# Optimization experiments

Measured on AMD Instinct MI355X. Metric: run time of the kernel, lower is better.

## Reference

```python
import jax, jax.numpy as jnp
from jax import lax
import numpy as np

NUM_NODES = 4
C = 256
P = 64
TOTAL_EDGES = sum(n + 1 for n in range(NUM_NODES))  # 10
STRENGTH = 1.0
W_SCALE = 0.02  # scale on raw randn weights to keep cascaded convs numerically tame


def setup_inputs() -> dict:
    key = jax.random.key(0)
    ks = jax.random.split(key, 16)
    rng = np.random.default_rng(0)
    idx = jnp.asarray(
        np.stack([rng.permutation(C)[:P] for _ in range(TOTAL_EDGES)]), dtype=jnp.int32
    )
    return {
        "x": jax.random.normal(ks[0], (64, C, 32, 32), jnp.float32),
        "arch_params": jax.random.normal(ks[1], (NUM_NODES, NUM_NODES + 1, 12), jnp.float32),
        "edge_norms": jnp.ones((NUM_NODES, NUM_NODES + 1), jnp.float32),
        "idx": idx,
        "w3": jax.random.normal(ks[2], (TOTAL_EDGES, P, P, 3, 3), jnp.float32) * W_SCALE,
        "w5": jax.random.normal(ks[3], (TOTAL_EDGES, P, P, 5, 5), jnp.float32) * W_SCALE,
        "w7": jax.random.normal(ks[4], (TOTAL_EDGES, P, P, 7, 7), jnp.float32) * W_SCALE,
        "w1": jax.random.normal(ks[5], (TOTAL_EDGES, P, P, 1, 1), jnp.float32) * W_SCALE,
        "sep3_dw": jax.random.normal(ks[6], (TOTAL_EDGES, P, 1, 3, 3), jnp.float32) * W_SCALE,
        "sep3_pw": jax.random.normal(ks[7], (TOTAL_EDGES, P, P, 1, 1), jnp.float32) * W_SCALE,
        "sep5_dw": jax.random.normal(ks[8], (TOTAL_EDGES, P, 1, 5, 5), jnp.float32) * W_SCALE,
        "sep5_pw": jax.random.normal(ks[9], (TOTAL_EDGES, P, P, 1, 1), jnp.float32) * W_SCALE,
        "dil3": jax.random.normal(ks[10], (TOTAL_EDGES, P, P, 3, 3), jnp.float32) * W_SCALE,
        "dil5": jax.random.normal(ks[11], (TOTAL_EDGES, P, P, 5, 5), jnp.float32) * W_SCALE,
    }


def _conv(x, w, pad, dil=1, groups=1):
    return lax.conv_general_dilated(
        x, w, window_strides=(1, 1), padding=[(pad, pad), (pad, pad)],
        rhs_dilation=(dil, dil), feature_group_count=groups,
        dimension_numbers=("NCHW", "OIHW", "NCHW"))


def _maxpool3(x):
    return lax.reduce_window(x, -jnp.inf, lax.max, (1, 1, 3, 3), (1, 1, 1, 1),
                             [(0, 0), (0, 0), (1, 1), (1, 1)])


def _avgpool3(x):  # count_include_pad=True (torch default) -> always /9
    s = lax.reduce_window(x, 0.0, lax.add, (1, 1, 3, 3), (1, 1, 1, 1),
                          [(0, 0), (0, 0), (1, 1), (1, 1)])
    return s / 9.0


def _forward(x, arch_params, edge_norms, idx, w3, w5, w7, w1,
             sep3_dw, sep3_pw, sep5_dw, sep5_pw, dil3, dil5):
    states = [x]
    e = 0
    for node in range(NUM_NODES):
        acc = jnp.zeros_like(x)
        for i in range(node + 1):
            s = states[i]
            norm = jnp.clip(edge_norms[node, i], 1e-5)
            w = jax.nn.softmax(arch_params[node, i] / norm ** STRENGTH)
            ids = idx[e]
            xs = s[:, ids]  # [B, P, H, W] gather of sampled channels
            # partial-channel ops (identity + convs); op 11 is ZeroOp -> no contribution
            p = w[0] * xs
            p = p + w[1] * _conv(xs, w3[e], 1)
            p = p + w[2] * _conv(xs, w5[e], 2)
            p = p + w[3] * _conv(xs, w7[e], 3)
            p = p + w[4] * _conv(xs, w1[e], 0)
            p = p + w[7] * _conv(_conv(xs, sep3_dw[e], 1, groups=P), sep3_pw[e], 0)
            p = p + w[8] * _conv(_conv(xs, sep5_dw[e], 2, groups=P), sep5_pw[e], 0)
            p = p + w[9] * _conv(xs, dil3[e], 2, dil=2)
            p = p + w[10] * _conv(xs, dil5[e], 4, dil=2)
            # full-channel pool ops
            acc = acc + w[5] * _maxpool3(s) + w[6] * _avgpool3(s)
            # scatter weighted partial sum back into full channel space
            acc = acc.at[:, ids].add(p)
            e += 1
        states.append(acc)
    return states[-1]


def reference(x, arch_params, edge_norms, idx, w3, w5, w7, w1,
              sep3_dw, sep3_pw, sep5_dw, sep5_pw, dil3, dil5):
    return _forward(x, arch_params, edge_norms, idx, w3, w5, w7, w1,
                    sep3_dw, sep3_pw, sep5_dw, sep5_pw, dil3, dil5)
```

## Files before the change

kernel.cpp:

```cpp
#include <hip/hip_runtime.h>
#include <math.h>


#define NB 64
#define CF 256
#define PC 64
#define HW 32
#define NEDGE 10
#define TAPS 81

#define TR 16
#define TC 40
#define CSTR 40
#define ROWSTR (TC * CSTR)

typedef _Float16 f16x8 __attribute__((ext_vector_type(8)));
typedef _Float16 f16x2 __attribute__((ext_vector_type(2)));
typedef float f32x4 __attribute__((ext_vector_type(4)));

__global__ void softmax_kernel(const float* __restrict__ arch,
                               const float* __restrict__ norms,
                               float* __restrict__ sw) {
    int e = threadIdx.x;
    if (e >= NEDGE) return;
    int node = 0, i = e;
    while (i > node) { i -= node + 1; node++; }
    float norm = fmaxf(norms[node * 5 + i], 1e-5f);
    const float* a = arch + (node * 5 + i) * 12;
    float v[12];
    float m = -3.0e38f;
    for (int k = 0; k < 12; ++k) { v[k] = a[k] / norm; m = fmaxf(m, v[k]); }
    float ssum = 0.f;
    for (int k = 0; k < 12; ++k) { v[k] = expf(v[k] - m); ssum += v[k]; }
    float inv = 1.0f / ssum;
    for (int k = 0; k < 12; ++k) sw[e * 12 + k] = v[k] * inv;
}

__global__ void build_w(const float* __restrict__ w3, const float* __restrict__ w5,
                        const float* __restrict__ w7, const float* __restrict__ w1,
                        const float* __restrict__ s3dw, const float* __restrict__ s3pw,
                        const float* __restrict__ s5dw, const float* __restrict__ s5pw,
                        const float* __restrict__ d3, const float* __restrict__ d5,
                        const float* __restrict__ sw, _Float16* __restrict__ Wh) {
    int gid = blockIdx.x * 256 + threadIdx.x;
    int c32 = gid & 31;
    int o   = (gid >> 5) & 63;
    int g   = (gid >> 11) & 1;
    int t2  = gid >> 12;
    int tap = t2 % TAPS;
    int e   = t2 / TAPS;
    int c   = (g << 5) | c32;

    int dy = tap / 9 - 4, dx = tap % 9 - 4;
    const float* w = sw + e * 12;
    int eoc = (e * 64 + o) * 64 + c;
    int ec  = e * 64 + c;
    float val = 0.f;
    int ady = dy < 0 ? -dy : dy, adx = dx < 0 ? -dx : dx;
    if (ady <= 1 && adx <= 1) {
        val += w[1] * w3[eoc * 9 + (dy + 1) * 3 + (dx + 1)];
        val += w[7] * s3pw[eoc] * s3dw[ec * 9 + (dy + 1) * 3 + (dx + 1)];
    }
    if (ady <= 2 && adx <= 2) {
        val += w[2] * w5[eoc * 25 + (dy + 2) * 5 + (dx + 2)];
        val += w[8] * s5pw[eoc] * s5dw[ec * 25 + (dy + 2) * 5 + (dx + 2)];
        if (((dy | dx) & 1) == 0)
            val += w[9] * d3[eoc * 9 + (dy / 2 + 1) * 3 + (dx / 2 + 1)];
    }
    if (ady <= 3 && adx <= 3)
        val += w[3] * w7[eoc * 49 + (dy + 3) * 7 + (dx + 3)];
    if (((dy | dx) & 1) == 0)
        val += w[10] * d5[eoc * 25 + (dy / 2 + 2) * 5 + (dx / 2 + 2)];
    if (dy == 0 && dx == 0)
        val += w[4] * w1[eoc];
    Wh[gid] = (_Float16)val;
}

__global__ void pool_node(const float* __restrict__ s0, const float* __restrict__ s1,
                          const float* __restrict__ s2, const float* __restrict__ s3,
                          float* __restrict__ acc, const float* __restrict__ sw,
                          int ebase, int nedges) {
    int gid = blockIdx.x * 256 + threadIdx.x;
    int x0 = (gid & 3) << 3;
    int y  = (gid >> 2) & 31;
    size_t plane = (size_t)(gid >> 7);
    const float* states[4] = {s0, s1, s2, s3};
    float outv[8];
    #pragma unroll
    for (int j = 0; j < 8; ++j) outv[j] = 0.f;

    for (int i = 0; i < nedges; ++i) {
        const float* base = states[i] + (plane << 10);
        float colmax[10], colsum[10];
        #pragma unroll
        for (int j = 0; j < 10; ++j) { colmax[j] = -3.0e38f; colsum[j] = 0.f; }
        #pragma unroll
        for (int dr = -1; dr <= 1; ++dr) {
            int r = y + dr;
            if ((unsigned)r < 32u) {
                const float* rp = base + (r << 5);
                float vals[10];
                vals[0] = (x0 > 0) ? rp[x0 - 1] : 0.f;
                f32x4 m0 = *(const f32x4*)(rp + x0);
                f32x4 m1 = *(const f32x4*)(rp + x0 + 4);
                vals[1] = m0.x; vals[2] = m0.y; vals[3] = m0.z; vals[4] = m0.w;
                vals[5] = m1.x; vals[6] = m1.y; vals[7] = m1.z; vals[8] = m1.w;
                vals[9] = (x0 < 24) ? rp[x0 + 8] : 0.f;
                #pragma unroll
                for (int j = 0; j < 10; ++j) {
                    colsum[j] += vals[j];
                    colmax[j] = fmaxf(colmax[j], vals[j]);
                }
            }
        }
        if (x0 == 0)  colmax[0] = -3.0e38f;
        if (x0 == 24) colmax[9] = -3.0e38f;

        float wmax = sw[(ebase + i) * 12 + 5];
        float wavg = sw[(ebase + i) * 12 + 6] * (1.0f / 9.0f);
        #pragma unroll
        for (int j = 0; j < 8; ++j) {
            float mx = fmaxf(fmaxf(colmax[j], colmax[j + 1]), colmax[j + 2]);
            float sm = colsum[j] + colsum[j + 1] + colsum[j + 2];
            outv[j] += wmax * mx + wavg * sm;
        }
    }
    float* op = acc + (plane << 10) + (y << 5) + x0;
    ((f32x4*)op)[0] = (f32x4){outv[0], outv[1], outv[2], outv[3]};
    ((f32x4*)op)[1] = (f32x4){outv[4], outv[5], outv[6], outv[7]};
}

__global__ __launch_bounds__(256, 3) void conv_node(
    const float* __restrict__ s0, const float* __restrict__ s1,
    const float* __restrict__ s2, const float* __restrict__ s3,
    float* __restrict__ acc, const _Float16* __restrict__ Wh,
    const int* __restrict__ idxg, const float* __restrict__ sw, int ebase) {
    __shared__ __align__(16) _Float16 tile[TR * ROWSTR];

    int i = blockIdx.y;
    int e = ebase + i;
    const float* sarr[4] = {s0, s1, s2, s3};
    const float* s = sarr[i];
    int g = blockIdx.z;

    int t  = threadIdx.x;
    int qy = blockIdx.x & 3;
    int n  = blockIdx.x >> 2;
    int y0 = qy << 3;

    for (int l = t; l < TR * ROWSTR / 8; l += 256)
        ((f32x4*)tile)[l] = (f32x4){0.f, 0.f, 0.f, 0.f};

    int lane = t & 63;
    int wave = __builtin_amdgcn_readfirstlane(t >> 6);
    int aoff = ((lane & 15) << 5) + ((lane >> 4) << 3);
    int boff = (lane & 15) * CSTR + ((lane >> 4) << 3);

    int sx = t & 31;
    int cp = t >> 5;

    f32x4 a[4][4];
    #pragma unroll
    for (int k = 0; k < 4; ++k)
        #pragma unroll
        for (int p = 0; p < 4; ++p) a[k][p] = (f32x4){0.f, 0.f, 0.f, 0.f};

    const int* ide = idxg + e * PC;

    __syncthreads();

    #pragma unroll
    for (int sub = 0; sub < 2; ++sub) {
        int c2 = cp + (sub << 3);
        int ca = (g << 5) + (c2 << 1);
        const float* pa = s + (((size_t)n * CF + ide[ca]) << 10);
        const float* pb = s + (((size_t)n * CF + ide[ca + 1]) << 10);
        #pragma unroll
        for (int r = 0; r < TR; ++r) {
            int ys = y0 - 4 + r;
            if ((unsigned)ys < 32u) {
                f16x2 h = {(_Float16)pa[(ys << 5) + sx], (_Float16)pb[(ys << 5) + sx]};
                *(f16x2*)&tile[r * ROWSTR + (4 + sx) * CSTR + (c2 << 1)] = h;
            }
        }
    }
    __syncthreads();

    const _Float16* wg = Wh + ((size_t)(e * TAPS) * 2 + g) * 2048 + aoff;
    int tb = wave << 1;
    for (int dx = 0; dx < 9; ++dx) {
        const _Float16* wx = wg + dx * 4096;
        const _Float16* brow = tile + boff + dx * CSTR;
        f16x8 F[2][2];
        F[0][0] = *(const f16x8*)(brow + tb * ROWSTR);
        F[0][1] = *(const f16x8*)(brow + tb * ROWSTR + 16 * CSTR);
        #pragma unroll
        for (int dy = 0; dy < 9; ++dy) {
            int rB = tb + dy + 1;
            F[(dy + 1) & 1][0] = *(const f16x8*)(brow + rB * ROWSTR);
            F[(dy + 1) & 1][1] = *(const f16x8*)(brow + rB * ROWSTR + 16 * CSTR);
            const _Float16* wp = wx + dy * 9 * 4096;
            f16x8 A0 = *(const f16x8*)(wp);
            f16x8 A1 = *(const f16x8*)(wp + 512);
            f16x8 A2 = *(const f16x8*)(wp + 1024);
            f16x8 A3 = *(const f16x8*)(wp + 1536);
            a[0][0] = __builtin_amdgcn_mfma_f32_16x16x32_f16(A0, F[dy & 1][0], a[0][0], 0, 0, 0);
            a[1][0] = __builtin_amdgcn_mfma_f32_16x16x32_f16(A1, F[dy & 1][0], a[1][0], 0, 0, 0);
            a[2][0] = __builtin_amdgcn_mfma_f32_16x16x32_f16(A2, F[dy & 1][0], a[2][0], 0, 0, 0);
            a[3][0] = __builtin_amdgcn_mfma_f32_16x16x32_f16(A3, F[dy & 1][0], a[3][0], 0, 0, 0);
            a[0][1] = __builtin_amdgcn_mfma_f32_16x16x32_f16(A0, F[dy & 1][1], a[0][1], 0, 0, 0);
            a[1][1] = __builtin_amdgcn_mfma_f32_16x16x32_f16(A1, F[dy & 1][1], a[1][1], 0, 0, 0);
            a[2][1] = __builtin_amdgcn_mfma_f32_16x16x32_f16(A2, F[dy & 1][1], a[2][1], 0, 0, 0);
            a[3][1] = __builtin_amdgcn_mfma_f32_16x16x32_f16(A3, F[dy & 1][1], a[3][1], 0, 0, 0);
            a[0][2] = __builtin_amdgcn_mfma_f32_16x16x32_f16(A0, F[(dy + 1) & 1][0], a[0][2], 0, 0, 0);
            a[1][2] = __builtin_amdgcn_mfma_f32_16x16x32_f16(A1, F[(dy + 1) & 1][0], a[1][2], 0, 0, 0);
            a[2][2] = __builtin_amdgcn_mfma_f32_16x16x32_f16(A2, F[(dy + 1) & 1][0], a[2][2], 0, 0, 0);
            a[3][2] = __builtin_amdgcn_mfma_f32_16x16x32_f16(A3, F[(dy + 1) & 1][0], a[3][2], 0, 0, 0);
            a[0][3] = __builtin_amdgcn_mfma_f32_16x16x32_f16(A0, F[(dy + 1) & 1][1], a[0][3], 0, 0, 0);
            a[1][3] = __builtin_amdgcn_mfma_f32_16x16x32_f16(A1, F[(dy + 1) & 1][1], a[1][3], 0, 0, 0);
            a[2][3] = __builtin_amdgcn_mfma_f32_16x16x32_f16(A2, F[(dy + 1) & 1][1], a[2][3], 0, 0, 0);
            a[3][3] = __builtin_amdgcn_mfma_f32_16x16x32_f16(A3, F[(dy + 1) & 1][1], a[3][3], 0, 0, 0);
        }
    }

    if (g == 0) {
        float w0 = sw[e * 12];
        #pragma unroll
        for (int of = 0; of < 4; ++of) {
            #pragma unroll
            for (int j = 0; j < 4; ++j) {
                int o = (of << 4) + ((lane >> 4) << 2) + j;
                int ch = ide[o];
                size_t base = ((size_t)n * CF + ch) << 10;
                float* ap = acc + base;
                const float* sp = s + base;
                #pragma unroll
                for (int rs = 0; rs < 2; ++rs) {
                    int y = y0 + (wave << 1) + rs;
                    #pragma unroll
                    for (int cb = 0; cb < 2; ++cb) {
                        int off = (y << 5) + (cb << 4) + (lane & 15);
                        atomicAdd(ap + off, a[of][(rs << 1) + cb][j] + w0 * sp[off]);
                    }
                }
            }
        }
    } else {
        #pragma unroll
        for (int of = 0; of < 4; ++of) {
            #pragma unroll
            for (int j = 0; j < 4; ++j) {
                int o = (of << 4) + ((lane >> 4) << 2) + j;
                int ch = ide[o];
                float* ap = acc + (((size_t)n * CF + ch) << 10);
                #pragma unroll
                for (int rs = 0; rs < 2; ++rs) {
                    int y = y0 + (wave << 1) + rs;
                    #pragma unroll
                    for (int cb = 0; cb < 2; ++cb) {
                        int off = (y << 5) + (cb << 4) + (lane & 15);
                        atomicAdd(ap + off, a[of][(rs << 1) + cb][j]);
                    }
                }
            }
        }
    }
}

extern "C" void kernel_launch(void* const* d_in, const int* in_sizes, int n_in,
                              void* d_out, int out_size, void* d_ws, size_t ws_size,
                              hipStream_t stream) {
    const float* x    = (const float*)d_in[0];
    const float* arch = (const float*)d_in[1];
    const float* norms= (const float*)d_in[2];
    const int*   idx  = (const int*)d_in[3];
    const float* w3   = (const float*)d_in[4];
    const float* w5   = (const float*)d_in[5];
    const float* w7   = (const float*)d_in[6];
    const float* w1   = (const float*)d_in[7];
    const float* s3dw = (const float*)d_in[8];
    const float* s3pw = (const float*)d_in[9];
    const float* s5dw = (const float*)d_in[10];
    const float* s5pw = (const float*)d_in[11];
    const float* d3   = (const float*)d_in[12];
    const float* d5   = (const float*)d_in[13];
    float* out = (float*)d_out;

    const size_t S = (size_t)NB * CF * HW * HW;
    float* st1 = (float*)d_ws;
    float* st2 = st1 + S;
    float* st3 = st2 + S;
    _Float16* Wh = (_Float16*)(st3 + S);
    float* sw = (float*)(Wh + (size_t)NEDGE * TAPS * 2 * 2048);

    softmax_kernel<<<1, 64, 0, stream>>>(arch, norms, sw);
    build_w<<<(NEDGE * TAPS * 2 * 2048) / 256, 256, 0, stream>>>(
        w3, w5, w7, w1, s3dw, s3pw, s5dw, s5pw, d3, d5, sw, Wh);

    float* states[5] = {(float*)x, st1, st2, st3, out};
    for (int node = 0; node < 4; ++node) {
        int ebase = node * (node + 1) / 2;
        pool_node<<<(int)(S / 8 / 256), 256, 0, stream>>>(
            states[0], states[1], states[2], states[3],
            states[node + 1], sw, ebase, node + 1);
        conv_node<<<dim3(NB * 4, node + 1, 2), 256, 0, stream>>>(
            states[0], states[1], states[2], states[3],
            states[node + 1], Wh, idx, sw, ebase);
    }
}
```

Baseline: 1.115 ms.

## Template conv tile height; use taller 16-row strips for later nodes

```diff
diff --git a/kernel.cpp b/kernel.cpp
--- a/kernel.cpp
+++ b/kernel.cpp
@@ -9,7 +9,6 @@
 #define NEDGE 10
 #define TAPS 81
 
-#define TR 16
 #define TC 40
 #define CSTR 40
 #define ROWSTR (TC * CSTR)
@@ -130,12 +129,16 @@
     ((f32x4*)op)[1] = (f32x4){outv[4], outv[5], outv[6], outv[7]};
 }
 
-__global__ __launch_bounds__(256, 3) void conv_node(
+template <int WR>
+__global__ __launch_bounds__(256, WR == 2 ? 3 : 2) void conv_node(
     const float* __restrict__ s0, const float* __restrict__ s1,
     const float* __restrict__ s2, const float* __restrict__ s3,
     float* __restrict__ acc, const _Float16* __restrict__ Wh,
     const int* __restrict__ idxg, const float* __restrict__ sw, int ebase) {
-    __shared__ __align__(16) _Float16 tile[TR * ROWSTR];
+    constexpr int SR = 4 * WR;
+    constexpr int TRR = SR + 8;
+    constexpr int STRIPS = 32 / SR;
+    __shared__ __align__(16) _Float16 tile[TRR * ROWSTR];
 
     int i = blockIdx.y;
     int e = ebase + i;
@@ -144,11 +147,11 @@
     int g = blockIdx.z;
 
     int t  = threadIdx.x;
-    int qy = blockIdx.x & 3;
-    int n  = blockIdx.x >> 2;
-    int y0 = qy << 3;
-
-    for (int l = t; l < TR * ROWSTR / 8; l += 256)
+    int qy = blockIdx.x & (STRIPS - 1);
+    int n  = blockIdx.x / STRIPS;
+    int y0 = qy * SR;
+
+    for (int l = t; l < TRR * ROWSTR / 8; l += 256)
         ((f32x4*)tile)[l] = (f32x4){0.f, 0.f, 0.f, 0.f};
 
     int lane = t & 63;
@@ -159,11 +162,11 @@
     int sx = t & 31;
     int cp = t >> 5;
 
-    f32x4 a[4][4];
+    f32x4 a[4][2 * WR];
     #pragma unroll
     for (int k = 0; k < 4; ++k)
         #pragma unroll
-        for (int p = 0; p < 4; ++p) a[k][p] = (f32x4){0.f, 0.f, 0.f, 0.f};
+        for (int p = 0; p < 2 * WR; ++p) a[k][p] = (f32x4){0.f, 0.f, 0.f, 0.f};
 
     const int* ide = idxg + e * PC;
 
@@ -176,7 +179,7 @@
         const float* pa = s + (((size_t)n * CF + ide[ca]) << 10);
         const float* pb = s + (((size_t)n * CF + ide[ca + 1]) << 10);
         #pragma unroll
-        for (int r = 0; r < TR; ++r) {
+        for (int r = 0; r < TRR; ++r) {
             int ys = y0 - 4 + r;
             if ((unsigned)ys < 32u) {
                 f16x2 h = {(_Float16)pa[(ys << 5) + sx], (_Float16)pb[(ys << 5) + sx]};
@@ -187,80 +190,63 @@
     __syncthreads();
 
     const _Float16* wg = Wh + ((size_t)(e * TAPS) * 2 + g) * 2048 + aoff;
-    int tb = wave << 1;
-    for (int dx = 0; dx < 9; ++dx) {
-        const _Float16* wx = wg + dx * 4096;
-        const _Float16* brow = tile + boff + dx * CSTR;
-        f16x8 F[2][2];
-        F[0][0] = *(const f16x8*)(brow + tb * ROWSTR);
-        F[0][1] = *(const f16x8*)(brow + tb * ROWSTR + 16 * CSTR);
-        #pragma unroll
-        for (int dy = 0; dy < 9; ++dy) {
-            int rB = tb + dy + 1;
-            F[(dy + 1) & 1][0] = *(const f16x8*)(brow + rB * ROWSTR);
-            F[(dy + 1) & 1][1] = *(const f16x8*)(brow + rB * ROWSTR + 16 * CSTR);
-            const _Float16* wp = wx + dy * 9 * 4096;
-            f16x8 A0 = *(const f16x8*)(wp);
-            f16x8 A1 = *(const f16x8*)(wp + 512);
-            f16x8 A2 = *(const f16x8*)(wp + 1024);
-            f16x8 A3 = *(const f16x8*)(wp + 1536);
-            a[0][0] = __builtin_amdgcn_mfma_f32_16x16x32_f16(A0, F[dy & 1][0], a[0][0], 0, 0, 0);
-            a[1][0] = __builtin_amdgcn_mfma_f32_16x16x32_f16(A1, F[dy & 1][0], a[1][0], 0, 0, 0);
-            a[2][0] = __builtin_amdgcn_mfma_f32_16x16x32_f16(A2, F[dy & 1][0], a[2][0], 0, 0, 0);
-            a[3][0] = __builtin_amdgcn_mfma_f32_16x16x32_f16(A3, F[dy & 1][0], a[3][0], 0, 0, 0);
-            a[0][1] = __builtin_amdgcn_mfma_f32_16x16x32_f16(A0, F[dy & 1][1], a[0][1], 0, 0, 0);
-            a[1][1] = __builtin_amdgcn_mfma_f32_16x16x32_f16(A1, F[dy & 1][1], a[1][1], 0, 0, 0);
-            a[2][1] = __builtin_amdgcn_mfma_f32_16x16x32_f16(A2, F[dy & 1][1], a[2][1], 0, 0, 0);
-            a[3][1] = __builtin_amdgcn_mfma_f32_16x16x32_f16(A3, F[dy & 1][1], a[3][1], 0, 0, 0);
-            a[0][2] = __builtin_amdgcn_mfma_f32_16x16x32_f16(A0, F[(dy + 1) & 1][0], a[0][2], 0, 0, 0);
-            a[1][2] = __builtin_amdgcn_mfma_f32_16x16x32_f16(A1, F[(dy + 1) & 1][0], a[1][2], 0, 0, 0);
-            a[2][2] = __builtin_amdgcn_mfma_f32_16x16x32_f16(A2, F[(dy + 1) & 1][0], a[2][2], 0, 0, 0);
-            a[3][2] = __builtin_amdgcn_mfma_f32_16x16x32_f16(A3, F[(dy + 1) & 1][0], a[3][2], 0, 0, 0);
-            a[0][3] = __builtin_amdgcn_mfma_f32_16x16x32_f16(A0, F[(dy + 1) & 1][1], a[0][3], 0, 0, 0);
-            a[1][3] = __builtin_amdgcn_mfma_f32_16x16x32_f16(A1, F[(dy + 1) & 1][1], a[1][3], 0, 0, 0);
-            a[2][3] = __builtin_amdgcn_mfma_f32_16x16x32_f16(A2, F[(dy + 1) & 1][1], a[2][3], 0, 0, 0);
-            a[3][3] = __builtin_amdgcn_mfma_f32_16x16x32_f16(A3, F[(dy + 1) & 1][1], a[3][3], 0, 0, 0);
-        }
-    }
-
-    if (g == 0) {
-        float w0 = sw[e * 12];
-        #pragma unroll
-        for (int of = 0; of < 4; ++of) {
+    const _Float16* bt = tile + boff;
+    int tb = wave * WR;
+
+    f16x8 F[WR][2];
+    #pragma unroll
+    for (int tp = 0; tp < 81; ++tp) {
+        const int dx = tp / 9, dy = tp % 9;
+        const _Float16* wp = wg + (dy * 9 + dx) * 4096;
+        f16x8 A0 = *(const f16x8*)(wp);
+        f16x8 A1 = *(const f16x8*)(wp + 512);
+        f16x8 A2 = *(const f16x8*)(wp + 1024);
+        f16x8 A3 = *(const f16x8*)(wp + 1536);
+        const _Float16* brow = bt + dx * CSTR;
+        if (dy == 0) {
             #pragma unroll
-            for (int j = 0; j < 4; ++j) {
-                int o = (of << 4) + ((lane >> 4) << 2) + j;
-                int ch = ide[o];
-                size_t base = ((size_t)n * CF + ch) << 10;
-                float* ap = acc + base;
-                const float* sp = s + base;
+            for (int m = 0; m < WR - 1; ++m) {
+                F[m & (WR - 1)][0] = *(const f16x8*)(brow + (tb + m) * ROWSTR);
+                F[m & (WR - 1)][1] = *(const f16x8*)(brow + (tb + m) * ROWSTR + 16 * CSTR);
+            }
+        }
+        {
+            const int m = dy + WR - 1;
+            F[m & (WR - 1)][0] = *(const f16x8*)(brow + (tb + m) * ROWSTR);
+            F[m & (WR - 1)][1] = *(const f16x8*)(brow + (tb + m) * ROWSTR + 16 * CSTR);
+        }
+        #pragma unroll
+        for (int k = 0; k < WR; ++k) {
+            #pragma unroll
+            for (int cb = 0; cb < 2; ++cb) {
+                const int sl = (dy + k) & (WR - 1);
+                a[0][2 * k + cb] = __builtin_amdgcn_mfma_f32_16x16x32_f16(A0, F[sl][cb], a[0][2 * k + cb], 0, 0, 0);
+                a[1][2 * k + cb] = __builtin_amdgcn_mfma_f32_16x16x32_f16(A1, F[sl][cb], a[1][2 * k + cb], 0, 0, 0);
+                a[2][2 * k + cb] = __builtin_amdgcn_mfma_f32_16x16x32_f16(A2, F[sl][cb], a[2][2 * k + cb], 0, 0, 0);
+                a[3][2 * k + cb] = __builtin_amdgcn_mfma_f32_16x16x32_f16(A3, F[sl][cb], a[3][2 * k + cb], 0, 0, 0);
+            }
+        }
+    }
+
+    float w0 = (g == 0) ? sw[e * 12] : 0.f;
+    #pragma unroll
+    for (int of = 0; of < 4; ++of) {
+        #pragma unroll
+        for (int j = 0; j < 4; ++j) {
+            int o = (of << 4) + ((lane >> 4) << 2) + j;
+            int ch = ide[o];
+            size_t base = ((size_t)n * CF + ch) << 10;
+            float* ap = acc + base;
+            const float* sp = s + base;
+            #pragma unroll
+            for (int k = 0; k < WR; ++k) {
+                int y = y0 + wave * WR + k;
                 #pragma unroll
-                for (int rs = 0; rs < 2; ++rs) {
-                    int y = y0 + (wave << 1) + rs;
-                    #pragma unroll
-                    for (int cb = 0; cb < 2; ++cb) {
-                        int off = (y << 5) + (cb << 4) + (lane & 15);
-                        atomicAdd(ap + off, a[of][(rs << 1) + cb][j] + w0 * sp[off]);
-                    }
-                }
-            }
-        }
-    } else {
-        #pragma unroll
-        for (int of = 0; of < 4; ++of) {
-            #pragma unroll
-            for (int j = 0; j < 4; ++j) {
-                int o = (of << 4) + ((lane >> 4) << 2) + j;
-                int ch = ide[o];
-                float* ap = acc + (((size_t)n * CF + ch) << 10);
-                #pragma unroll
-                for (int rs = 0; rs < 2; ++rs) {
-                    int y = y0 + (wave << 1) + rs;
-                    #pragma unroll
-                    for (int cb = 0; cb < 2; ++cb) {
-                        int off = (y << 5) + (cb << 4) + (lane & 15);
-                        atomicAdd(ap + off, a[of][(rs << 1) + cb][j]);
-                    }
+                for (int cb = 0; cb < 2; ++cb) {
+                    int off = (y << 5) + (cb << 4) + (lane & 15);
+                    float v = a[of][2 * k + cb][j];
+                    if (g == 0) v += w0 * sp[off];
+                    atomicAdd(ap + off, v);
                 }
             }
         }
@@ -303,8 +289,14 @@
         pool_node<<<(int)(S / 8 / 256), 256, 0, stream>>>(
             states[0], states[1], states[2], states[3],
             states[node + 1], sw, ebase, node + 1);
-        conv_node<<<dim3(NB * 4, node + 1, 2), 256, 0, stream>>>(
-            states[0], states[1], states[2], states[3],
-            states[node + 1], Wh, idx, sw, ebase);
-    }
-}
+        if (node == 0) {
+            conv_node<2><<<dim3(NB * 4, 1, 2), 256, 0, stream>>>(
+                states[0], states[1], states[2], states[3],
+                states[1], Wh, idx, sw, ebase);
+        } else {
+            conv_node<4><<<dim3(NB * 2, node + 1, 2), 256, 0, stream>>>(
+                states[0], states[1], states[2], states[3],
+                states[node + 1], Wh, idx, sw, ebase);
+        }
+    }
+}
```

Measured after the change: 1.110 ms. No clear change (-0.4%).
